# Kernel optimization log

Measured on AMD Instinct MI355X. Metric: run time of the kernel, lower is better.

## Reference

```python
import jax, jax.numpy as jnp
import numpy as np

HIDDEN = 512
BATCH = 128
SEQ = 512


def setup_inputs() -> dict:
    key = jax.random.key(0)
    k_ins, k_res, k1, k2, k3, k4 = jax.random.split(key, 6)
    bound = 1.0 / np.sqrt(HIDDEN)  # torch GRUCell default init
    u = lambda k, shape: jax.random.uniform(k, shape, jnp.float32, -bound, bound)
    return {
        "hidden": jnp.zeros((BATCH, HIDDEN), jnp.float32),
        "ins": jax.random.normal(k_ins, (BATCH, SEQ, HIDDEN), jnp.float32),
        "resets": jax.random.randint(k_res, (BATCH, SEQ), 0, 2).astype(jnp.bool_),
        "W_ih": u(k1, (3 * HIDDEN, HIDDEN)),
        "W_hh": u(k2, (3 * HIDDEN, HIDDEN)),
        "b_ih": u(k3, (3 * HIDDEN,)),
        "b_hh": u(k4, (3 * HIDDEN,)),
    }


def reference(hidden, ins, resets, W_ih, W_hh, b_ih, b_hh):
    # PyTorch GRUCell gate order: reset, update, new
    def step(h, xt):
        x, rmask = xt  # x: [B,H], rmask: [B]
        h = jnp.where(rmask[:, None], jnp.zeros_like(h), h)  # reset carry
        gi = x @ W_ih.T + b_ih   # [B, 3H]
        gh = h @ W_hh.T + b_hh   # [B, 3H]
        i_r, i_z, i_n = jnp.split(gi, 3, axis=-1)
        h_r, h_z, h_n = jnp.split(gh, 3, axis=-1)
        r = jax.nn.sigmoid(i_r + h_r)
        z = jax.nn.sigmoid(i_z + h_z)
        n = jnp.tanh(i_n + r * h_n)
        h_new = (1.0 - z) * n + z * h
        return h_new, h_new

    xs = (jnp.swapaxes(ins, 0, 1), jnp.swapaxes(resets, 0, 1))  # time-major
    h_final, ys = jax.lax.scan(step, hidden, xs)
    return h_final, jnp.swapaxes(ys, 0, 1)  # outputs back to [B,T,H]
```

## Files before the change

### kernel.cpp

```cpp
#include <hip/hip_runtime.h>
#include <hip/hip_bf16.h>
#include <stdint.h>

#define T_SEQ 512
#define HID   512
#define BATCH 128
#define G_B   8
#define G_N   32
#define BB    (BATCH / G_B)
#define HC    (HID / G_N)
#define NROW  (3 * HC)
#define HFIN  (BATCH * HID)
#define WSTR  512
#define XSTR  520
#define GSTR  20

using f32x4  = __attribute__((ext_vector_type(4))) float;
using short8 = __attribute__((ext_vector_type(8))) short;
using bfs4   = __attribute__((ext_vector_type(4))) short;

typedef const __attribute__((address_space(1))) void* gas_t;
typedef __attribute__((address_space(3))) void* las_t;

__device__ __forceinline__ short8 pack8(float a0, float a1, float a2, float a3,
                                        float a4, float a5, float a6, float a7) {
    union { uint32_t u[4]; short8 s; } r;
    asm("v_cvt_pk_bf16_f32 %0, %1, %2" : "=v"(r.u[0]) : "v"(a0), "v"(a1));
    asm("v_cvt_pk_bf16_f32 %0, %1, %2" : "=v"(r.u[1]) : "v"(a2), "v"(a3));
    asm("v_cvt_pk_bf16_f32 %0, %1, %2" : "=v"(r.u[2]) : "v"(a4), "v"(a5));
    asm("v_cvt_pk_bf16_f32 %0, %1, %2" : "=v"(r.u[3]) : "v"(a6), "v"(a7));
    return r.s;
}

__device__ __forceinline__ uint16_t f2bf(float f) {
    uint32_t u = __builtin_bit_cast(uint32_t, f);
    return (uint16_t)((u + 0x7fffu + ((u >> 16) & 1u)) >> 16);
}

__device__ __forceinline__ int lws(int row, int ko) {
    return row * WSTR + (ko ^ ((row & 7) << 3));
}

__global__ void __launch_bounds__(128, 1) gru_scan(
    const float* __restrict__ hidden,
    const float* __restrict__ ins,
    const int*   __restrict__ resets,
    const float* __restrict__ W_ih,
    const float* __restrict__ W_hh,
    const float* __restrict__ b_ih,
    const float* __restrict__ b_hh,
    float* __restrict__ out,
    uint32_t* __restrict__ flags,
    unsigned short* __restrict__ xbs)
{
    __shared__ __align__(16) short ldsW[2][NROW * WSTR];
    __shared__ __align__(16) float ldsX[BB * XSTR];
    __shared__ __align__(16) float giB[64 * GSTR];
    __shared__ __align__(16) float hnvB[64 * 4];

    const int wg   = blockIdx.x;
    const int bb   = wg & 7;
    const int nn   = wg >> 3;
    const int tid  = threadIdx.x;
    const int lane = tid & 63;
    const int wv   = tid >> 6;
    const int l15  = lane & 15;
    const int lg   = lane >> 4;

#define STAGE_X(T_) do {                                                      \
        _Pragma("unroll")                                                     \
        for (int i_ = 0; i_ < 32; ++i_) {                                     \
            const int r_ = i_ >> 1, hf_ = i_ & 1;                             \
            const float* src_ = ins + ((size_t)(bb * BB + r_) * T_SEQ + (T_)) \
                                   * HID + hf_ * 256 + lane * 4;              \
            float* dst_ = (float*)&ldsX[r_ * XSTR + hf_ * 256];               \
            __builtin_amdgcn_global_load_lds((gas_t)src_, (las_t)dst_,        \
                                             16, 0, 0);                       \
        }                                                                     \
    } while (0)

    if (wv) STAGE_X(0);

    for (int idx = tid; idx < NROW * (HID / 4); idx += 128) {
        const int row = idx >> 7;
        const int k4  = (idx & 127) << 2;
        const int g   = row >> 4;
        const int i   = row & 15;
        const int grow = g * HID + nn * HC + i;
        f32x4 wi = *(const f32x4*)&W_ih[(size_t)grow * HID + k4];
        f32x4 wh = *(const f32x4*)&W_hh[(size_t)grow * HID + k4];
        bfs4 si = { (short)f2bf(wi[0]), (short)f2bf(wi[1]), (short)f2bf(wi[2]), (short)f2bf(wi[3]) };
        bfs4 sh = { (short)f2bf(wh[0]), (short)f2bf(wh[1]), (short)f2bf(wh[2]), (short)f2bf(wh[3]) };
        *(bfs4*)&ldsW[0][lws(row, k4)] = si;
        *(bfs4*)&ldsW[1][lws(row, k4)] = sh;
    }
    __syncthreads();

    const int arow  = bb * BB + l15;
    const int drow0 = bb * BB + lg * 4;
    const int dcol  = nn * HC + l15;
    float* const ys = out + HFIN;

    if (wv) {
        for (int t = 0; t < T_SEQ; ++t) {
            asm volatile("s_waitcnt vmcnt(0)" ::: "memory");
            __builtin_amdgcn_sched_barrier(0);

            short8 af[16];
            const float* xr = &ldsX[l15 * XSTR + lg * 8];
            #pragma unroll
            for (int kt = 0; kt < 16; ++kt) {
                f32x4 x0 = *(const f32x4*)(xr + kt * 32);
                f32x4 x1 = *(const f32x4*)(xr + kt * 32 + 4);
                af[kt] = pack8(x0[0], x0[1], x0[2], x0[3], x1[0], x1[1], x1[2], x1[3]);
            }

            f32x4 aIr = {0,0,0,0}, aIz = {0,0,0,0}, aIn = {0,0,0,0};
            #pragma unroll
            for (int kt = 0; kt < 16; ++kt) {
                const int ko = kt * 32 + lg * 8;
                aIr = __builtin_amdgcn_mfma_f32_16x16x32_bf16(af[kt], *(const short8*)&ldsW[0][lws(l15, ko)], aIr, 0, 0, 0);
                aIz = __builtin_amdgcn_mfma_f32_16x16x32_bf16(af[kt], *(const short8*)&ldsW[0][lws(16 + l15, ko)], aIz, 0, 0, 0);
                aIn = __builtin_amdgcn_mfma_f32_16x16x32_bf16(af[kt], *(const short8*)&ldsW[0][lws(32 + l15, ko)], aIn, 0, 0, 0);
            }
            *(f32x4*)&giB[lane * GSTR + 0] = aIr;
            *(f32x4*)&giB[lane * GSTR + 4] = aIz;
            *(f32x4*)&giB[lane * GSTR + 8] = aIn;
            asm volatile("s_waitcnt lgkmcnt(0)" ::: "memory");
            __builtin_amdgcn_s_barrier();
            if (t + 1 < T_SEQ) STAGE_X(t + 1);
            __builtin_amdgcn_s_barrier();

            f32x4 hn = *(const f32x4*)&hnvB[lane * 4];
            #pragma unroll
            for (int j = 0; j < 4; ++j) {
                const int r_ = drow0 + j;
                ys[((size_t)r_ * T_SEQ + t) * HID + dcol] = hn[j];
                if (t == T_SEQ - 1) out[(size_t)r_ * HID + dcol] = hn[j];
            }
        }
    } else {
        const float bir = b_ih[dcol], biz = b_ih[HID + dcol], bin_ = b_ih[2 * HID + dcol];
        const float bhr = b_hh[dcol], bhz = b_hh[HID + dcol], bhn  = b_hh[2 * HID + dcol];

        float hprev[4];
        #pragma unroll
        for (int j = 0; j < 4; ++j)
            hprev[j] = hidden[(size_t)(drow0 + j) * HID + dcol];

        const uint32_t* fp = flags + bb * 32 + (lane & 31);
        uint32_t* const fme = flags + bb * 32 + nn;

        for (int t = 0; t < T_SEQ; ++t) {
            short8 ah[16];
            int rstA, rstD[4];
            rstA = resets[(size_t)arow * T_SEQ + t];
            #pragma unroll
            for (int j = 0; j < 4; ++j)
                rstD[j] = resets[(size_t)(drow0 + j) * T_SEQ + t];

            if (t == 0) {
                const float* hrow = hidden + (size_t)arow * HID + lg * 8;
                const float am = rstA ? 0.f : 1.f;
                #pragma unroll
                for (int kt = 0; kt < 16; ++kt) {
                    f32x4 h0 = *(const f32x4*)(hrow + kt * 32);
                    f32x4 h1 = *(const f32x4*)(hrow + kt * 32 + 4);
                    ah[kt] = pack8(am * h0[0], am * h0[1], am * h0[2], am * h0[3],
                                   am * h1[0], am * h1[1], am * h1[2], am * h1[3]);
                }
            } else {
                uint32_t f;
                do {
                    asm volatile("global_load_dword %0, %1, off sc0 sc1\n\t"
                                 "s_waitcnt vmcnt(0)"
                                 : "=v"(f) : "v"(fp) : "memory");
                } while (!__all((int)(f >= (uint32_t)t)));
                __builtin_amdgcn_sched_barrier(0);

                const unsigned short* hb = xbs + (size_t)((t - 1) & 1) * HFIN
                                               + (size_t)arow * HID + lg * 8;
#define LOADH(K, OFFS) \
    asm volatile("global_load_dwordx4 %0, %1, off offset:" OFFS " sc0 sc1" \
                 : "=v"(ah[K]) : "v"(hb) : "memory")
                LOADH(0, "0");    LOADH(1, "64");   LOADH(2, "128");  LOADH(3, "192");
                LOADH(4, "256");  LOADH(5, "320");  LOADH(6, "384");  LOADH(7, "448");
                LOADH(8, "512");  LOADH(9, "576");  LOADH(10, "640"); LOADH(11, "704");
                LOADH(12, "768"); LOADH(13, "832"); LOADH(14, "896"); LOADH(15, "960");
#undef LOADH
                asm volatile("s_waitcnt vmcnt(0)" ::: "memory");
                __builtin_amdgcn_sched_barrier(0);
                if (rstA) {
                    const short8 z8 = {0,0,0,0,0,0,0,0};
                    #pragma unroll
                    for (int kt = 0; kt < 16; ++kt) ah[kt] = z8;
                }
            }

            __builtin_amdgcn_s_barrier();

            f32x4 aIr = *(const f32x4*)&giB[lane * GSTR + 0];
            f32x4 aIz = *(const f32x4*)&giB[lane * GSTR + 4];
            f32x4 aIn = *(const f32x4*)&giB[lane * GSTR + 8];

            f32x4 aHr = {0,0,0,0}, aHz = {0,0,0,0}, aHn = {0,0,0,0};
            #pragma unroll
            for (int kt = 0; kt < 16; ++kt) {
                const int ko = kt * 32 + lg * 8;
                aHr = __builtin_amdgcn_mfma_f32_16x16x32_bf16(ah[kt], *(const short8*)&ldsW[1][lws(l15, ko)], aHr, 0, 0, 0);
                aHz = __builtin_amdgcn_mfma_f32_16x16x32_bf16(ah[kt], *(const short8*)&ldsW[1][lws(16 + l15, ko)], aHz, 0, 0, 0);
                aHn = __builtin_amdgcn_mfma_f32_16x16x32_bf16(ah[kt], *(const short8*)&ldsW[1][lws(32 + l15, ko)], aHn, 0, 0, 0);
            }

            f32x4 hv;
            #pragma unroll
            for (int j = 0; j < 4; ++j) {
                const float hp = rstD[j] ? 0.f : hprev[j];
                const float gr = aIr[j] + bir + aHr[j] + bhr;
                const float rg = 1.f / (1.f + __expf(-gr));
                const float gz = aIz[j] + biz + aHz[j] + bhz;
                const float zg = 1.f / (1.f + __expf(-gz));
                float gn = aIn[j] + bin_ + rg * (aHn[j] + bhn);
                gn = fminf(fmaxf(gn, -15.f), 15.f);
                const float e2 = __expf(2.f * gn);
                const float ng = (e2 - 1.f) / (e2 + 1.f);
                const float hn = (1.f - zg) * ng + zg * hp;
                hprev[j] = hn;
                hv[j] = hn;
            }
            *(f32x4*)&hnvB[lane * 4] = hv;

            if (t < T_SEQ - 1) {
                #pragma unroll
                for (int j = 0; j < 4; ++j) {
                    uint32_t v = f2bf(hv[j]);
                    unsigned short* p = xbs + (size_t)(t & 1) * HFIN
                                            + (size_t)(drow0 + j) * HID + dcol;
                    asm volatile("global_store_short %0, %1, off sc0 sc1"
                                 :: "v"(p), "v"(v) : "memory");
                }
                asm volatile("s_waitcnt vmcnt(0)" ::: "memory");
                if (lane == 0) {
                    uint32_t tag = (uint32_t)(t + 1);
                    asm volatile("global_store_dword %0, %1, off sc0 sc1"
                                 :: "v"(fme), "v"(tag) : "memory");
                }
            }
            asm volatile("s_waitcnt lgkmcnt(0)" ::: "memory");
            __builtin_amdgcn_s_barrier();
        }
    }
#undef STAGE_X
}

extern "C" void kernel_launch(void* const* d_in, const int* in_sizes, int n_in,
                              void* d_out, int out_size, void* d_ws, size_t ws_size,
                              hipStream_t stream) {
    const float* hidden = (const float*)d_in[0];
    const float* ins    = (const float*)d_in[1];
    const int*   resets = (const int*)d_in[2];
    const float* W_ih   = (const float*)d_in[3];
    const float* W_hh   = (const float*)d_in[4];
    const float* b_ih   = (const float*)d_in[5];
    const float* b_hh   = (const float*)d_in[6];
    float* out = (float*)d_out;
    uint32_t* flags = (uint32_t*)d_ws;
    unsigned short* xbs = (unsigned short*)((char*)d_ws + 1024);

    hipMemsetAsync(flags, 0, 1024, stream);
    gru_scan<<<dim3(G_B * G_N), dim3(128), 0, stream>>>(
        hidden, ins, resets, W_ih, W_hh, b_ih, b_hh, out, flags, xbs);
}
```

Measured before the change: 1.720 ms.

## Replace per-block flag handshake with step-tagged hidden-state words

Each bf16 hidden value is now stored in a 32-bit word whose upper half carries the step tag. Consumers poll the data itself until every tag matches, so the separate flag poll, the store-then-wait fence and the flag write are gone. This removes one cross-block round-trip per timestep from the serial chain. In exchange the hidden exchange traffic doubles, each poll iteration reloads the full row, and the memset grows to cover the tagged buffers.

```diff
diff --git a/kernel.cpp b/kernel.cpp
--- a/kernel.cpp
+++ b/kernel.cpp
@@ -18,6 +18,7 @@
 using f32x4  = __attribute__((ext_vector_type(4))) float;
 using short8 = __attribute__((ext_vector_type(8))) short;
 using bfs4   = __attribute__((ext_vector_type(4))) short;
+using u32x4  = __attribute__((ext_vector_type(4))) unsigned int;
 
 typedef const __attribute__((address_space(1))) void* gas_t;
 typedef __attribute__((address_space(3))) void* las_t;
@@ -50,8 +51,7 @@
     const float* __restrict__ b_ih,
     const float* __restrict__ b_hh,
     float* __restrict__ out,
-    uint32_t* __restrict__ flags,
-    unsigned short* __restrict__ xbs)
+    uint32_t* __restrict__ xb)
 {
     __shared__ __align__(16) short ldsW[2][NROW * WSTR];
     __shared__ __align__(16) float ldsX[BB * XSTR];
@@ -148,17 +148,14 @@
         for (int j = 0; j < 4; ++j)
             hprev[j] = hidden[(size_t)(drow0 + j) * HID + dcol];
 
-        const uint32_t* fp = flags + bb * 32 + (lane & 31);
-        uint32_t* const fme = flags + bb * 32 + nn;
-
         for (int t = 0; t < T_SEQ; ++t) {
-            short8 ah[16];
             int rstA, rstD[4];
             rstA = resets[(size_t)arow * T_SEQ + t];
             #pragma unroll
             for (int j = 0; j < 4; ++j)
                 rstD[j] = resets[(size_t)(drow0 + j) * T_SEQ + t];
 
+            short8 ah[16];
             if (t == 0) {
                 const float* hrow = hidden + (size_t)arow * HID + lg * 8;
                 const float am = rstA ? 0.f : 1.f;
@@ -170,26 +167,47 @@
                                    am * h1[0], am * h1[1], am * h1[2], am * h1[3]);
                 }
             } else {
-                uint32_t f;
-                do {
-                    asm volatile("global_load_dword %0, %1, off sc0 sc1\n\t"
-                                 "s_waitcnt vmcnt(0)"
-                                 : "=v"(f) : "v"(fp) : "memory");
-                } while (!__all((int)(f >= (uint32_t)t)));
+                const uint32_t wtag = (uint32_t)t << 16;
+                const uint32_t* hb = xb + (size_t)((t - 1) & 1) * HFIN
+                                        + (size_t)arow * HID + lg * 8;
+                u32x4 d[32];
+#define PL(K, O0, O1) \
+    asm volatile("global_load_dwordx4 %0, %2, off offset:" O0 " sc0 sc1\n\t" \
+                 "global_load_dwordx4 %1, %2, off offset:" O1 " sc0 sc1" \
+                 : "=v"(d[2*K]), "=v"(d[2*K+1]) : "v"(hb) : "memory")
+                for (;;) {
+                    PL(0,  "0",    "16");   PL(1,  "128",  "144");
+                    PL(2,  "256",  "272");  PL(3,  "384",  "400");
+                    PL(4,  "512",  "528");  PL(5,  "640",  "656");
+                    PL(6,  "768",  "784");  PL(7,  "896",  "912");
+                    PL(8,  "1024", "1040"); PL(9,  "1152", "1168");
+                    PL(10, "1280", "1296"); PL(11, "1408", "1424");
+                    PL(12, "1536", "1552"); PL(13, "1664", "1680");
+                    PL(14, "1792", "1808"); PL(15, "1920", "1936");
+                    asm volatile("s_waitcnt vmcnt(0)" ::: "memory");
+                    __builtin_amdgcn_sched_barrier(0);
+                    uint32_t bad = 0;
+                    #pragma unroll
+                    for (int q = 0; q < 32; ++q) {
+                        bad |= (d[q][0] ^ wtag) & 0xffff0000u;
+                        bad |= (d[q][1] ^ wtag) & 0xffff0000u;
+                        bad |= (d[q][2] ^ wtag) & 0xffff0000u;
+                        bad |= (d[q][3] ^ wtag) & 0xffff0000u;
+                    }
+                    if (!__any((int)(bad != 0))) break;
+                    __builtin_amdgcn_s_sleep(1);
+                }
+#undef PL
                 __builtin_amdgcn_sched_barrier(0);
-
-                const unsigned short* hb = xbs + (size_t)((t - 1) & 1) * HFIN
-                                               + (size_t)arow * HID + lg * 8;
-#define LOADH(K, OFFS) \
-    asm volatile("global_load_dwordx4 %0, %1, off offset:" OFFS " sc0 sc1" \
-                 : "=v"(ah[K]) : "v"(hb) : "memory")
-                LOADH(0, "0");    LOADH(1, "64");   LOADH(2, "128");  LOADH(3, "192");
-                LOADH(4, "256");  LOADH(5, "320");  LOADH(6, "384");  LOADH(7, "448");
-                LOADH(8, "512");  LOADH(9, "576");  LOADH(10, "640"); LOADH(11, "704");
-                LOADH(12, "768"); LOADH(13, "832"); LOADH(14, "896"); LOADH(15, "960");
-#undef LOADH
-                asm volatile("s_waitcnt vmcnt(0)" ::: "memory");
-                __builtin_amdgcn_sched_barrier(0);
+                #pragma unroll
+                for (int kt = 0; kt < 16; ++kt) {
+                    union { uint32_t w[4]; short8 s; } r;
+                    r.w[0] = __builtin_amdgcn_perm(d[2*kt][1],   d[2*kt][0],   0x05040100u);
+                    r.w[1] = __builtin_amdgcn_perm(d[2*kt][3],   d[2*kt][2],   0x05040100u);
+                    r.w[2] = __builtin_amdgcn_perm(d[2*kt+1][1], d[2*kt+1][0], 0x05040100u);
+                    r.w[3] = __builtin_amdgcn_perm(d[2*kt+1][3], d[2*kt+1][2], 0x05040100u);
+                    ah[kt] = r.s;
+                }
                 if (rstA) {
                     const short8 z8 = {0,0,0,0,0,0,0,0};
                     #pragma unroll
@@ -227,25 +245,16 @@
                 const float hn = (1.f - zg) * ng + zg * hp;
                 hprev[j] = hn;
                 hv[j] = hn;
-            }
+                if (t < T_SEQ - 1) {
+                    uint32_t v = ((uint32_t)(t + 1) << 16) | f2bf(hn);
+                    uint32_t* p = xb + (size_t)(t & 1) * HFIN
+                                     + (size_t)(drow0 + j) * HID + dcol;
+                    asm volatile("global_store_dword %0, %1, off sc0 sc1"
+                                 :: "v"(p), "v"(v) : "memory");
+                }
+            }
+
             *(f32x4*)&hnvB[lane * 4] = hv;
-
-            if (t < T_SEQ - 1) {
-                #pragma unroll
-                for (int j = 0; j < 4; ++j) {
-                    uint32_t v = f2bf(hv[j]);
-                    unsigned short* p = xbs + (size_t)(t & 1) * HFIN
-                                            + (size_t)(drow0 + j) * HID + dcol;
-                    asm volatile("global_store_short %0, %1, off sc0 sc1"
-                                 :: "v"(p), "v"(v) : "memory");
-                }
-                asm volatile("s_waitcnt vmcnt(0)" ::: "memory");
-                if (lane == 0) {
-                    uint32_t tag = (uint32_t)(t + 1);
-                    asm volatile("global_store_dword %0, %1, off sc0 sc1"
-                                 :: "v"(fme), "v"(tag) : "memory");
-                }
-            }
             asm volatile("s_waitcnt lgkmcnt(0)" ::: "memory");
             __builtin_amdgcn_s_barrier();
         }
@@ -264,10 +273,9 @@
     const float* b_ih   = (const float*)d_in[5];
     const float* b_hh   = (const float*)d_in[6];
     float* out = (float*)d_out;
-    uint32_t* flags = (uint32_t*)d_ws;
-    unsigned short* xbs = (unsigned short*)((char*)d_ws + 1024);
-
-    hipMemsetAsync(flags, 0, 1024, stream);
+    uint32_t* xb = (uint32_t*)d_ws;
+
+    hipMemsetAsync(xb, 0, (size_t)2 * HFIN * 4, stream);
     gru_scan<<<dim3(G_B * G_N), dim3(128), 0, stream>>>(
-        hidden, ins, resets, W_ih, W_hh, b_ih, b_hh, out, flags, xbs);
-}
+        hidden, ins, resets, W_ih, W_hh, b_ih, b_hh, out, xb);
+}
```

Measured after the change: 2.860 ms. +66.3%, slower.

## Hold bf16 weight fragments in registers and preload resets into LDS

Applied to the files above, without the earlier changes.

Each wave now loads its GRU weight slice (W_ih for the input wave, W_hh for the recurrent wave) straight from global memory into 48 bf16 registers, replacing the swizzled LDS weight tiles. This removes LDS weight reads from the per-step MFMA loops on the serial critical path. The reset mask is transposed into LDS once up front instead of being read from global memory every step. Each h value's global store is now issued right after it is computed, and the hnvB write moves after the flag publish. The large register footprint (192 VGPRs for weights) risks spills or pressure.

```diff
diff --git a/kernel.cpp b/kernel.cpp
--- a/kernel.cpp
+++ b/kernel.cpp
@@ -9,15 +9,13 @@
 #define G_N   32
 #define BB    (BATCH / G_B)
 #define HC    (HID / G_N)
-#define NROW  (3 * HC)
 #define HFIN  (BATCH * HID)
-#define WSTR  512
-#define XSTR  520
+#define XSTR  516
 #define GSTR  20
 
 using f32x4  = __attribute__((ext_vector_type(4))) float;
 using short8 = __attribute__((ext_vector_type(8))) short;
-using bfs4   = __attribute__((ext_vector_type(4))) short;
+using u32x4  = __attribute__((ext_vector_type(4))) unsigned int;
 
 typedef const __attribute__((address_space(1))) void* gas_t;
 typedef __attribute__((address_space(3))) void* las_t;
@@ -35,10 +33,6 @@
 __device__ __forceinline__ uint16_t f2bf(float f) {
     uint32_t u = __builtin_bit_cast(uint32_t, f);
     return (uint16_t)((u + 0x7fffu + ((u >> 16) & 1u)) >> 16);
-}
-
-__device__ __forceinline__ int lws(int row, int ko) {
-    return row * WSTR + (ko ^ ((row & 7) << 3));
 }
 
 __global__ void __launch_bounds__(128, 1) gru_scan(
@@ -53,8 +47,8 @@
     uint32_t* __restrict__ flags,
     unsigned short* __restrict__ xbs)
 {
-    __shared__ __align__(16) short ldsW[2][NROW * WSTR];
     __shared__ __align__(16) float ldsX[BB * XSTR];
+    __shared__ __align__(16) int   ldsR[T_SEQ * BB];
     __shared__ __align__(16) float giB[64 * GSTR];
     __shared__ __align__(16) float hnvB[64 * 4];
 
@@ -81,18 +75,30 @@
 
     if (wv) STAGE_X(0);
 
-    for (int idx = tid; idx < NROW * (HID / 4); idx += 128) {
-        const int row = idx >> 7;
-        const int k4  = (idx & 127) << 2;
-        const int g   = row >> 4;
-        const int i   = row & 15;
-        const int grow = g * HID + nn * HC + i;
-        f32x4 wi = *(const f32x4*)&W_ih[(size_t)grow * HID + k4];
-        f32x4 wh = *(const f32x4*)&W_hh[(size_t)grow * HID + k4];
-        bfs4 si = { (short)f2bf(wi[0]), (short)f2bf(wi[1]), (short)f2bf(wi[2]), (short)f2bf(wi[3]) };
-        bfs4 sh = { (short)f2bf(wh[0]), (short)f2bf(wh[1]), (short)f2bf(wh[2]), (short)f2bf(wh[3]) };
-        *(bfs4*)&ldsW[0][lws(row, k4)] = si;
-        *(bfs4*)&ldsW[1][lws(row, k4)] = sh;
+    for (int idx = tid; idx < BB * (T_SEQ / 4); idx += 128) {
+        const int r  = idx >> 7;
+        const int t4 = (idx & 127) << 2;
+        u32x4 v = *(const u32x4*)&resets[(size_t)(bb * BB + r) * T_SEQ + t4];
+        ldsR[(t4 + 0) * BB + r] = (int)v[0];
+        ldsR[(t4 + 1) * BB + r] = (int)v[1];
+        ldsR[(t4 + 2) * BB + r] = (int)v[2];
+        ldsR[(t4 + 3) * BB + r] = (int)v[3];
+    }
+
+    short8 wreg[48];
+    {
+        const float* Ws = wv ? W_ih : W_hh;
+        #pragma unroll
+        for (int g = 0; g < 3; ++g) {
+            const float* base = Ws + (size_t)(g * HID + nn * HC + l15) * HID + lg * 8;
+            #pragma unroll
+            for (int kt = 0; kt < 16; ++kt) {
+                f32x4 w0 = *(const f32x4*)(base + kt * 32);
+                f32x4 w1 = *(const f32x4*)(base + kt * 32 + 4);
+                wreg[g * 16 + kt] = pack8(w0[0], w0[1], w0[2], w0[3],
+                                          w1[0], w1[1], w1[2], w1[3]);
+            }
+        }
     }
     __syncthreads();
 
@@ -118,10 +124,9 @@
             f32x4 aIr = {0,0,0,0}, aIz = {0,0,0,0}, aIn = {0,0,0,0};
             #pragma unroll
             for (int kt = 0; kt < 16; ++kt) {
-                const int ko = kt * 32 + lg * 8;
-                aIr = __builtin_amdgcn_mfma_f32_16x16x32_bf16(af[kt], *(const short8*)&ldsW[0][lws(l15, ko)], aIr, 0, 0, 0);
-                aIz = __builtin_amdgcn_mfma_f32_16x16x32_bf16(af[kt], *(const short8*)&ldsW[0][lws(16 + l15, ko)], aIz, 0, 0, 0);
-                aIn = __builtin_amdgcn_mfma_f32_16x16x32_bf16(af[kt], *(const short8*)&ldsW[0][lws(32 + l15, ko)], aIn, 0, 0, 0);
+                aIr = __builtin_amdgcn_mfma_f32_16x16x32_bf16(af[kt], wreg[kt],      aIr, 0, 0, 0);
+                aIz = __builtin_amdgcn_mfma_f32_16x16x32_bf16(af[kt], wreg[16 + kt], aIz, 0, 0, 0);
+                aIn = __builtin_amdgcn_mfma_f32_16x16x32_bf16(af[kt], wreg[32 + kt], aIn, 0, 0, 0);
             }
             *(f32x4*)&giB[lane * GSTR + 0] = aIr;
             *(f32x4*)&giB[lane * GSTR + 4] = aIz;
@@ -152,13 +157,13 @@
         uint32_t* const fme = flags + bb * 32 + nn;
 
         for (int t = 0; t < T_SEQ; ++t) {
+            const int rstA = ldsR[t * BB + l15];
+            int rstD[4];
+            #pragma unroll
+            for (int j = 0; j < 4; ++j)
+                rstD[j] = ldsR[t * BB + lg * 4 + j];
+
             short8 ah[16];
-            int rstA, rstD[4];
-            rstA = resets[(size_t)arow * T_SEQ + t];
-            #pragma unroll
-            for (int j = 0; j < 4; ++j)
-                rstD[j] = resets[(size_t)(drow0 + j) * T_SEQ + t];
-
             if (t == 0) {
                 const float* hrow = hidden + (size_t)arow * HID + lg * 8;
                 const float am = rstA ? 0.f : 1.f;
@@ -206,10 +211,9 @@
             f32x4 aHr = {0,0,0,0}, aHz = {0,0,0,0}, aHn = {0,0,0,0};
             #pragma unroll
             for (int kt = 0; kt < 16; ++kt) {
-                const int ko = kt * 32 + lg * 8;
-                aHr = __builtin_amdgcn_mfma_f32_16x16x32_bf16(ah[kt], *(const short8*)&ldsW[1][lws(l15, ko)], aHr, 0, 0, 0);
-                aHz = __builtin_amdgcn_mfma_f32_16x16x32_bf16(ah[kt], *(const short8*)&ldsW[1][lws(16 + l15, ko)], aHz, 0, 0, 0);
-                aHn = __builtin_amdgcn_mfma_f32_16x16x32_bf16(ah[kt], *(const short8*)&ldsW[1][lws(32 + l15, ko)], aHn, 0, 0, 0);
+                aHr = __builtin_amdgcn_mfma_f32_16x16x32_bf16(ah[kt], wreg[kt],      aHr, 0, 0, 0);
+                aHz = __builtin_amdgcn_mfma_f32_16x16x32_bf16(ah[kt], wreg[16 + kt], aHz, 0, 0, 0);
+                aHn = __builtin_amdgcn_mfma_f32_16x16x32_bf16(ah[kt], wreg[32 + kt], aHn, 0, 0, 0);
             }
 
             f32x4 hv;
@@ -227,18 +231,16 @@
                 const float hn = (1.f - zg) * ng + zg * hp;
                 hprev[j] = hn;
                 hv[j] = hn;
-            }
-            *(f32x4*)&hnvB[lane * 4] = hv;
-
-            if (t < T_SEQ - 1) {
-                #pragma unroll
-                for (int j = 0; j < 4; ++j) {
-                    uint32_t v = f2bf(hv[j]);
+                if (t < T_SEQ - 1) {
+                    uint32_t v = f2bf(hn);
                     unsigned short* p = xbs + (size_t)(t & 1) * HFIN
                                             + (size_t)(drow0 + j) * HID + dcol;
                     asm volatile("global_store_short %0, %1, off sc0 sc1"
                                  :: "v"(p), "v"(v) : "memory");
                 }
+            }
+
+            if (t < T_SEQ - 1) {
                 asm volatile("s_waitcnt vmcnt(0)" ::: "memory");
                 if (lane == 0) {
                     uint32_t tag = (uint32_t)(t + 1);
@@ -246,6 +248,8 @@
                                  :: "v"(fme), "v"(tag) : "memory");
                 }
             }
+
+            *(f32x4*)&hnvB[lane * 4] = hv;
             asm volatile("s_waitcnt lgkmcnt(0)" ::: "memory");
             __builtin_amdgcn_s_barrier();
         }
```

After: 1.804 ms. 4.9% more time.

## Consume hidden-state chunks incrementally as producer flags arrive, pad flags

Applied to the files above, without the earlier changes.

The recurrent step no longer waits for all 32 producer blocks before loading h. It polls the per-producer flags, loads each 32-wide K chunk as soon as both of its producers are ready, and issues the MFMAs for that chunk right away. Each flag is also padded to its own 256-byte slot to avoid false sharing between producers, and the hidden-state stores are moved earlier, before the LDS write. This overlaps the matmul with waiting on slow producers, at the cost of more polling iterations and branchy load code.

```diff
diff --git a/kernel.cpp b/kernel.cpp
--- a/kernel.cpp
+++ b/kernel.cpp
@@ -14,6 +14,7 @@
 #define WSTR  512
 #define XSTR  520
 #define GSTR  20
+#define FSTR  64
 
 using f32x4  = __attribute__((ext_vector_type(4))) float;
 using short8 = __attribute__((ext_vector_type(8))) short;
@@ -148,16 +149,17 @@
         for (int j = 0; j < 4; ++j)
             hprev[j] = hidden[(size_t)(drow0 + j) * HID + dcol];
 
-        const uint32_t* fp = flags + bb * 32 + (lane & 31);
-        uint32_t* const fme = flags + bb * 32 + nn;
+        const uint32_t* fp = flags + (size_t)(bb * 32 + (lane & 31)) * FSTR;
+        uint32_t* const fme = flags + (size_t)(bb * 32 + nn) * FSTR;
 
         for (int t = 0; t < T_SEQ; ++t) {
-            short8 ah[16];
             int rstA, rstD[4];
             rstA = resets[(size_t)arow * T_SEQ + t];
             #pragma unroll
             for (int j = 0; j < 4; ++j)
                 rstD[j] = resets[(size_t)(drow0 + j) * T_SEQ + t];
+
+            f32x4 aHr = {0,0,0,0}, aHz = {0,0,0,0}, aHn = {0,0,0,0};
 
             if (t == 0) {
                 const float* hrow = hidden + (size_t)arow * HID + lg * 8;
@@ -166,35 +168,69 @@
                 for (int kt = 0; kt < 16; ++kt) {
                     f32x4 h0 = *(const f32x4*)(hrow + kt * 32);
                     f32x4 h1 = *(const f32x4*)(hrow + kt * 32 + 4);
-                    ah[kt] = pack8(am * h0[0], am * h0[1], am * h0[2], am * h0[3],
-                                   am * h1[0], am * h1[1], am * h1[2], am * h1[3]);
+                    short8 ah = pack8(am * h0[0], am * h0[1], am * h0[2], am * h0[3],
+                                      am * h1[0], am * h1[1], am * h1[2], am * h1[3]);
+                    const int ko = kt * 32 + lg * 8;
+                    aHr = __builtin_amdgcn_mfma_f32_16x16x32_bf16(ah, *(const short8*)&ldsW[1][lws(l15, ko)], aHr, 0, 0, 0);
+                    aHz = __builtin_amdgcn_mfma_f32_16x16x32_bf16(ah, *(const short8*)&ldsW[1][lws(16 + l15, ko)], aHz, 0, 0, 0);
+                    aHn = __builtin_amdgcn_mfma_f32_16x16x32_bf16(ah, *(const short8*)&ldsW[1][lws(32 + l15, ko)], aHn, 0, 0, 0);
                 }
             } else {
-                uint32_t f;
+                const unsigned short* hb = xbs + (size_t)((t - 1) & 1) * HFIN
+                                               + (size_t)arow * HID + lg * 8;
+                short8 ah[16];
+                uint32_t done = 0;
                 do {
+                    uint32_t f;
                     asm volatile("global_load_dword %0, %1, off sc0 sc1\n\t"
                                  "s_waitcnt vmcnt(0)"
                                  : "=v"(f) : "v"(fp) : "memory");
-                } while (!__all((int)(f >= (uint32_t)t)));
-                __builtin_amdgcn_sched_barrier(0);
-
-                const unsigned short* hb = xbs + (size_t)((t - 1) & 1) * HFIN
-                                               + (size_t)arow * HID + lg * 8;
+                    const uint64_t rdy64 = __ballot((int)(f >= (uint32_t)t));
+                    const uint32_t rdy = (uint32_t)rdy64;
+                    uint32_t newk = 0;
+                    #pragma unroll
+                    for (int kt = 0; kt < 16; ++kt)
+                        if (((rdy >> (2 * kt)) & 3u) == 3u) newk |= (1u << kt);
+                    newk &= ~done;
+                    if (newk == 0) continue;
 #define LOADH(K, OFFS) \
     asm volatile("global_load_dwordx4 %0, %1, off offset:" OFFS " sc0 sc1" \
                  : "=v"(ah[K]) : "v"(hb) : "memory")
-                LOADH(0, "0");    LOADH(1, "64");   LOADH(2, "128");  LOADH(3, "192");
-                LOADH(4, "256");  LOADH(5, "320");  LOADH(6, "384");  LOADH(7, "448");
-                LOADH(8, "512");  LOADH(9, "576");  LOADH(10, "640"); LOADH(11, "704");
-                LOADH(12, "768"); LOADH(13, "832"); LOADH(14, "896"); LOADH(15, "960");
+                    if (newk & (1u << 0))  LOADH(0, "0");
+                    if (newk & (1u << 1))  LOADH(1, "64");
+                    if (newk & (1u << 2))  LOADH(2, "128");
+                    if (newk & (1u << 3))  LOADH(3, "192");
+                    if (newk & (1u << 4))  LOADH(4, "256");
+                    if (newk & (1u << 5))  LOADH(5, "320");
+                    if (newk & (1u << 6))  LOADH(6, "384");
+                    if (newk & (1u << 7))  LOADH(7, "448");
+                    if (newk & (1u << 8))  LOADH(8, "512");
+                    if (newk & (1u << 9))  LOADH(9, "576");
+                    if (newk & (1u << 10)) LOADH(10, "640");
+                    if (newk & (1u << 11)) LOADH(11, "704");
+                    if (newk & (1u << 12)) LOADH(12, "768");
+                    if (newk & (1u << 13)) LOADH(13, "832");
+                    if (newk & (1u << 14)) LOADH(14, "896");
+                    if (newk & (1u << 15)) LOADH(15, "960");
 #undef LOADH
-                asm volatile("s_waitcnt vmcnt(0)" ::: "memory");
-                __builtin_amdgcn_sched_barrier(0);
-                if (rstA) {
+                    asm volatile("s_waitcnt vmcnt(0)" ::: "memory");
+                    __builtin_amdgcn_sched_barrier(0);
                     const short8 z8 = {0,0,0,0,0,0,0,0};
-                    #pragma unroll
-                    for (int kt = 0; kt < 16; ++kt) ah[kt] = z8;
-                }
+#define DOKT(K) \
+    if (newk & (1u << K)) { \
+        short8 a_ = rstA ? z8 : ah[K]; \
+        const int ko_ = K * 32 + lg * 8; \
+        aHr = __builtin_amdgcn_mfma_f32_16x16x32_bf16(a_, *(const short8*)&ldsW[1][lws(l15, ko_)], aHr, 0, 0, 0); \
+        aHz = __builtin_amdgcn_mfma_f32_16x16x32_bf16(a_, *(const short8*)&ldsW[1][lws(16 + l15, ko_)], aHz, 0, 0, 0); \
+        aHn = __builtin_amdgcn_mfma_f32_16x16x32_bf16(a_, *(const short8*)&ldsW[1][lws(32 + l15, ko_)], aHn, 0, 0, 0); \
+    }
+                    DOKT(0)  DOKT(1)  DOKT(2)  DOKT(3)
+                    DOKT(4)  DOKT(5)  DOKT(6)  DOKT(7)
+                    DOKT(8)  DOKT(9)  DOKT(10) DOKT(11)
+                    DOKT(12) DOKT(13) DOKT(14) DOKT(15)
+#undef DOKT
+                    done |= newk;
+                } while (done != 0xFFFFu);
             }
 
             __builtin_amdgcn_s_barrier();
@@ -202,15 +238,6 @@
             f32x4 aIr = *(const f32x4*)&giB[lane * GSTR + 0];
             f32x4 aIz = *(const f32x4*)&giB[lane * GSTR + 4];
             f32x4 aIn = *(const f32x4*)&giB[lane * GSTR + 8];
-
-            f32x4 aHr = {0,0,0,0}, aHz = {0,0,0,0}, aHn = {0,0,0,0};
-            #pragma unroll
-            for (int kt = 0; kt < 16; ++kt) {
-                const int ko = kt * 32 + lg * 8;
-                aHr = __builtin_amdgcn_mfma_f32_16x16x32_bf16(ah[kt], *(const short8*)&ldsW[1][lws(l15, ko)], aHr, 0, 0, 0);
-                aHz = __builtin_amdgcn_mfma_f32_16x16x32_bf16(ah[kt], *(const short8*)&ldsW[1][lws(16 + l15, ko)], aHz, 0, 0, 0);
-                aHn = __builtin_amdgcn_mfma_f32_16x16x32_bf16(ah[kt], *(const short8*)&ldsW[1][lws(32 + l15, ko)], aHn, 0, 0, 0);
-            }
 
             f32x4 hv;
             #pragma unroll
@@ -227,18 +254,16 @@
                 const float hn = (1.f - zg) * ng + zg * hp;
                 hprev[j] = hn;
                 hv[j] = hn;
-            }
-            *(f32x4*)&hnvB[lane * 4] = hv;
-
-            if (t < T_SEQ - 1) {
-                #pragma unroll
-                for (int j = 0; j < 4; ++j) {
-                    uint32_t v = f2bf(hv[j]);
+                if (t < T_SEQ - 1) {
+                    uint32_t v = f2bf(hn);
                     unsigned short* p = xbs + (size_t)(t & 1) * HFIN
                                             + (size_t)(drow0 + j) * HID + dcol;
                     asm volatile("global_store_short %0, %1, off sc0 sc1"
                                  :: "v"(p), "v"(v) : "memory");
                 }
+            }
+
+            if (t < T_SEQ - 1) {
                 asm volatile("s_waitcnt vmcnt(0)" ::: "memory");
                 if (lane == 0) {
                     uint32_t tag = (uint32_t)(t + 1);
@@ -246,6 +271,8 @@
                                  :: "v"(fme), "v"(tag) : "memory");
                 }
             }
+
+            *(f32x4*)&hnvB[lane * 4] = hv;
             asm volatile("s_waitcnt lgkmcnt(0)" ::: "memory");
             __builtin_amdgcn_s_barrier();
         }
@@ -265,9 +292,9 @@
     const float* b_hh   = (const float*)d_in[6];
     float* out = (float*)d_out;
     uint32_t* flags = (uint32_t*)d_ws;
-    unsigned short* xbs = (unsigned short*)((char*)d_ws + 1024);
-
-    hipMemsetAsync(flags, 0, 1024, stream);
+    unsigned short* xbs = (unsigned short*)((char*)d_ws + 65536);
+
+    hipMemsetAsync(flags, 0, 65536, stream);
     gru_scan<<<dim3(G_B * G_N), dim3(128), 0, stream>>>(
         hidden, ins, resets, W_ih, W_hh, b_ih, b_hh, out, flags, xbs);
 }
```

New measurement: 2.358 ms. 1.37x slower.
